# Performance work log

Hardware: AMD Instinct MI355X
Metric: run time of the kernel (lower is better)

## Reference

```python
import jax, jax.numpy as jnp
import numpy as np
from jax import lax

M, N, D = 4096, 4096, 256
SINKHORN_ITERATIONS = 100
SINKHORN_EPSILON = 0.1
DESC_SCALE = 0.05  # keep exp(S/eps) finite for random descriptors


def setup_inputs() -> dict:
    key = jax.random.key(0)
    k1, k2 = jax.random.split(key)
    d_M_q = jax.random.normal(k1, (M, D), dtype=jnp.float32) * DESC_SCALE
    d_N_r = jax.random.normal(k2, (N, D), dtype=jnp.float32) * DESC_SCALE
    z = jnp.float32(0.5)  # SuperGlue bin_score default
    return {"d_M_q": d_M_q, "d_N_r": d_N_r, "z": z}


def reference(d_M_q, d_N_r, z):
    m, n = d_M_q.shape[0], d_N_r.shape[0]
    # score matrix [M, N]
    S = jnp.einsum('md,nd->mn', d_M_q, d_N_r)
    # augment with dustbin row/col filled with z -> [M+1, N+1]
    dtype = d_M_q.dtype
    last_col = jnp.full((m, 1), z, dtype=dtype)
    last_row = jnp.full((1, n + 1), z, dtype=dtype)
    S_aug = jnp.concatenate([jnp.concatenate([S, last_col], axis=1), last_row], axis=0)
    K = jnp.exp(S_aug / SINKHORN_EPSILON)

    def step(K, _):
        K = K / K.sum(axis=1, keepdims=True)  # row normalize
        K = K / K.sum(axis=0, keepdims=True)  # col normalize
        return K, None

    K, _ = lax.scan(step, K, None, length=SINKHORN_ITERATIONS)
    P = K[:m, :n]
    return P, K
```

## Files before the change

### kernel.cpp

```cpp
#include <hip/hip_runtime.h>
#include <hip/hip_bf16.h>


#define MROWS 4096
#define NCOLS 4096
#define DDIM 256
#define MP1 4097
#define INV_EPS 10.0f
#define NBLK 256
#define XSLOT 4160
#define BAR_DW 160

typedef __attribute__((ext_vector_type(8))) short bf16x8;
typedef __attribute__((ext_vector_type(4))) float f32x4;
typedef __attribute__((ext_vector_type(2))) float f32x2;
typedef __attribute__((ext_vector_type(4))) unsigned short u16x4;

static __device__ __forceinline__ unsigned short f2bf(float f) {
  __hip_bfloat16 h = __float2bfloat16(f);
  union { __hip_bfloat16 h; unsigned short s; } c;
  c.h = h;
  return c.s;
}

static __device__ __forceinline__ void ld_strip(const float* ps, float4& xv) {
  asm volatile("global_load_dwordx4 %0, %1, off sc0 sc1\n\t"
               "s_waitcnt vmcnt(0)"
               : "=v"(xv) : "v"(ps) : "memory");
}
static __device__ __forceinline__ void ld_strip_dust(const float* ps, const float* pd,
                                                     float4& xv, float& xd) {
  asm volatile("global_load_dwordx4 %0, %2, off sc0 sc1\n\t"
               "global_load_dword %1, %3, off sc0 sc1\n\t"
               "s_waitcnt vmcnt(0)"
               : "=v"(xv), "=v"(xd)
               : "v"(ps), "v"(pd)
               : "memory");
}
static __device__ __forceinline__ void st_coherent(float* p, float x) {
  asm volatile("global_store_dword %0, %1, off sc0 sc1" :: "v"(p), "v"(x) : "memory");
}
static __device__ __forceinline__ unsigned ld_flagc(const unsigned* p) {
  unsigned r;
  asm volatile("global_load_dword %0, %1, off sc0 sc1\n\t"
               "s_waitcnt vmcnt(0)"
               : "=v"(r) : "v"(p) : "memory");
  return r;
}
static __device__ __forceinline__ void st_flag(unsigned* p, unsigned x) {
  asm volatile("global_store_dword %0, %1, off sc0 sc1" :: "v"(p), "v"(x) : "memory");
}

template <int MODE>
__global__ __launch_bounds__(256) void mfma_gemm_kernel(
    const float* __restrict__ Q, const float* __restrict__ R,
    unsigned char* __restrict__ A8, unsigned char* __restrict__ T8,
    float* __restrict__ Kf, float* __restrict__ P,
    const float* __restrict__ u, const float* __restrict__ v)
{
  __shared__ unsigned short Qs[128][40];
  __shared__ unsigned short Rs[128][40];

  const int tid = threadIdx.x;
  const int lane = tid & 63;
  const int wid = tid >> 6;
  const int wy = wid >> 1;
  const int wx = wid & 1;
  const int rb = blockIdx.y * 128;
  const int cb = blockIdx.x * 128;
  const int lr = tid >> 3;
  const int lf = (tid & 7) * 4;

  f32x4 acc[4][4];
#pragma unroll
  for (int m = 0; m < 4; ++m)
#pragma unroll
    for (int n = 0; n < 4; ++n)
      acc[m][n] = (f32x4){0.f, 0.f, 0.f, 0.f};

  for (int k0 = 0; k0 < DDIM; k0 += 32) {
    float4 qv[4], rv[4];
#pragma unroll
    for (int i = 0; i < 4; ++i) {
      qv[i] = *reinterpret_cast<const float4*>(&Q[(size_t)(rb + lr + 32 * i) * DDIM + k0 + lf]);
      rv[i] = *reinterpret_cast<const float4*>(&R[(size_t)(cb + lr + 32 * i) * DDIM + k0 + lf]);
    }
    __syncthreads();
#pragma unroll
    for (int i = 0; i < 4; ++i) {
      u16x4 qs = {f2bf(qv[i].x), f2bf(qv[i].y), f2bf(qv[i].z), f2bf(qv[i].w)};
      u16x4 rs = {f2bf(rv[i].x), f2bf(rv[i].y), f2bf(rv[i].z), f2bf(rv[i].w)};
      *reinterpret_cast<u16x4*>(&Qs[lr + 32 * i][lf]) = qs;
      *reinterpret_cast<u16x4*>(&Rs[lr + 32 * i][lf]) = rs;
    }
    __syncthreads();

    const int ko = (lane >> 4) * 8;
    const int fr = lane & 15;
    bf16x8 af[4], bg[4];
#pragma unroll
    for (int m = 0; m < 4; ++m)
      af[m] = *reinterpret_cast<const bf16x8*>(&Qs[wy * 64 + m * 16 + fr][ko]);
#pragma unroll
    for (int n = 0; n < 4; ++n)
      bg[n] = *reinterpret_cast<const bf16x8*>(&Rs[wx * 64 + n * 16 + fr][ko]);
#pragma unroll
    for (int m = 0; m < 4; ++m)
#pragma unroll
      for (int n = 0; n < 4; ++n)
        acc[m][n] = __builtin_amdgcn_mfma_f32_16x16x32_bf16(af[m], bg[n], acc[m][n], 0, 0, 0);
  }

  const int r0 = (lane >> 4) * 4;
  const int fc = lane & 15;
#pragma unroll
  for (int m = 0; m < 4; ++m) {
    const int row0 = rb + wy * 64 + m * 16 + r0;
    float uu[4];
    if (MODE == 1) {
#pragma unroll
      for (int r = 0; r < 4; ++r) uu[r] = u[row0 + r];
    }
#pragma unroll
    for (int n = 0; n < 4; ++n) {
      const int col = cb + wx * 64 + n * 16 + fc;
      if (MODE == 0) {
        float kv[4];
#pragma unroll
        for (int r = 0; r < 4; ++r) kv[r] = __expf(acc[m][n][r] * INV_EPS);
        int packed = __builtin_amdgcn_cvt_pk_fp8_f32(kv[0], kv[1], 0, false);
        packed = __builtin_amdgcn_cvt_pk_fp8_f32(kv[2], kv[3], packed, true);
        *reinterpret_cast<unsigned int*>(&T8[(size_t)col * NCOLS + row0]) = (unsigned int)packed;
#pragma unroll
        for (int r = 0; r < 4; ++r)
          A8[(size_t)(row0 + r) * NCOLS + col] = (unsigned char)(((unsigned int)packed >> (8 * r)) & 0xffu);
      } else {
        const float vc = v[col];
#pragma unroll
        for (int r = 0; r < 4; ++r) {
          const float kv = __expf(acc[m][n][r] * INV_EPS);
          const float val = uu[r] * kv * vc;
          Kf[(size_t)(row0 + r) * MP1 + col] = val;
          P[(size_t)(row0 + r) * NCOLS + col] = val;
        }
      }
    }
  }
}

__global__ void init_sync_kernel(float* __restrict__ xbuf, unsigned* __restrict__ bar)
{
  const int i = blockIdx.x * 1024 + threadIdx.x;
  if (i < MP1) xbuf[i] = 1.0f;
  if (i < BAR_DW) bar[i] = 0u;
}

__global__ void edgeK_kernel(const float* __restrict__ zp, float* __restrict__ Kf,
                             const float* __restrict__ u, const float* __restrict__ v)
{
  const int i = blockIdx.x * 256 + threadIdx.x;
  if (i >= MP1) return;
  const float E = __expf(zp[0] * INV_EPS);
  Kf[(size_t)i * MP1 + NCOLS] = u[i] * E * v[NCOLS];
  Kf[(size_t)MROWS * MP1 + i] = u[MROWS] * E * v[i];
}

__global__ __launch_bounds__(1024) void sinkhorn_persist_kernel(
    const unsigned char* __restrict__ A8, const unsigned char* __restrict__ T8,
    float* __restrict__ xbuf, const float* __restrict__ zp,
    unsigned* __restrict__ bar)
{
  __shared__ unsigned char lA[16 * 4096];
  __shared__ unsigned char lT[16 * 4096];
  __shared__ float scratch[2][16][17];
  __shared__ float dscr[2][16];

  const int tid = threadIdx.x;
  const int b = blockIdx.x;
  const int lane = tid & 63;
  const int w = tid >> 6;
  const float E = __expf(zp[0] * INV_EPS);
  const int rev4 = ((lane & 1) << 3) | ((lane & 2) << 1) | ((lane & 4) >> 1) | ((lane & 8) >> 3);

  unsigned* cg = bar + ((b & 7) << 4);
  unsigned* release = bar + 128;

  {
    const uint4* gA = reinterpret_cast<const uint4*>(A8 + (size_t)b * 16 * 4096);
    const uint4* gT = reinterpret_cast<const uint4*>(T8 + (size_t)b * 16 * 4096);
    uint4* sA = reinterpret_cast<uint4*>(lA);
    uint4* sT = reinterpret_cast<uint4*>(lT);
#pragma unroll
    for (int i = 0; i < 4; ++i) {
      sA[tid + 1024 * i] = gA[tid + 1024 * i];
      sT[tid + 1024 * i] = gT[tid + 1024 * i];
    }
  }
  __syncthreads();

  const int c0 = (w << 8) + (lane << 2);

  for (int g = 1; g <= 200; ++g) {
    const unsigned char* Kl = (g & 1) ? lA : lT;
    const float* xin = xbuf + (size_t)((g - 1) & 3) * XSLOT;
    float* xout = xbuf + (size_t)(g & 3) * XSLOT;
    const unsigned need = (unsigned)(g - 1);
    const int sb = g & 1;

    if (w == 0) {
      unsigned fv = ld_flagc(release + (lane & 7));
      while (!__all((int)(fv >= need))) {
        __builtin_amdgcn_s_sleep(1);
        fv = ld_flagc(release + (lane & 7));
      }
    }
    __syncthreads();

    float4 xv; float xd = 0.f;
    if (w == 0) ld_strip_dust(xin + c0, xin + 4096, xv, xd);
    else        ld_strip(xin + c0, xv);

    float acc[16];
#pragma unroll
    for (int r = 0; r < 16; ++r) {
      const unsigned int aw = *reinterpret_cast<const unsigned int*>(Kl + r * 4096 + c0);
      const f32x2 lo = __builtin_amdgcn_cvt_pk_f32_fp8((int)aw, false);
      const f32x2 hi = __builtin_amdgcn_cvt_pk_f32_fp8((int)aw, true);
      acc[r] = lo.x * xv.x + lo.y * xv.y + hi.x * xv.z + hi.y * xv.w;
    }

    float r8[8], r4[4], r2[2], r1;
    {
      const bool f0 = (lane & 1) != 0;
#pragma unroll
      for (int k = 0; k < 8; ++k) {
        const float send = f0 ? acc[k] : acc[k + 8];
        const float keep = f0 ? acc[k + 8] : acc[k];
        r8[k] = keep + __shfl_xor(send, 1, 64);
      }
      const bool f1 = (lane & 2) != 0;
#pragma unroll
      for (int k = 0; k < 4; ++k) {
        const float send = f1 ? r8[k] : r8[k + 4];
        const float keep = f1 ? r8[k + 4] : r8[k];
        r4[k] = keep + __shfl_xor(send, 2, 64);
      }
      const bool f2 = (lane & 4) != 0;
#pragma unroll
      for (int k = 0; k < 2; ++k) {
        const float send = f2 ? r4[k] : r4[k + 2];
        const float keep = f2 ? r4[k + 2] : r4[k];
        r2[k] = keep + __shfl_xor(send, 4, 64);
      }
      const bool f3 = (lane & 8) != 0;
      {
        const float send = f3 ? r2[0] : r2[1];
        const float keep = f3 ? r2[1] : r2[0];
        r1 = keep + __shfl_xor(send, 8, 64);
      }
      r1 += __shfl_xor(r1, 16, 64);
      r1 += __shfl_xor(r1, 32, 64);
    }
    if (lane < 16) scratch[sb][rev4][w] = r1;

    if (b == 0) {
      float sv = xv.x + xv.y + xv.z + xv.w;
      sv += __shfl_xor(sv, 1, 64);  sv += __shfl_xor(sv, 2, 64);
      sv += __shfl_xor(sv, 4, 64);  sv += __shfl_xor(sv, 8, 64);
      sv += __shfl_xor(sv, 16, 64); sv += __shfl_xor(sv, 32, 64);
      if (lane == 0) dscr[sb][w] = sv;
    }
    __syncthreads();

    if (w == 0) {
      const int rr = lane >> 2, wq = (lane & 3) * 4;
      float s = scratch[sb][rr][wq] + scratch[sb][rr][wq + 1]
              + scratch[sb][rr][wq + 2] + scratch[sb][rr][wq + 3];
      s += __shfl_xor(s, 1, 64);
      s += __shfl_xor(s, 2, 64);
      if ((lane & 3) == 0)
        st_coherent(xout + (b << 4) + rr, 1.0f / (s + E * xd));
      if (b == 0) {
        float t = (lane < 16) ? dscr[sb][lane] : 0.f;
        t += __shfl_xor(t, 1, 64);  t += __shfl_xor(t, 2, 64);
        t += __shfl_xor(t, 4, 64);  t += __shfl_xor(t, 8, 64);
        t += __shfl_xor(t, 16, 64); t += __shfl_xor(t, 32, 64);
        if (lane == 0) st_coherent(xout + 4096, 1.0f / (E * (t + xd)));
      }
      asm volatile("s_waitcnt vmcnt(0)" ::: "memory");
      if (lane == 0) {
        const unsigned a = __hip_atomic_fetch_add(cg, 1u, __ATOMIC_RELAXED,
                                                  __HIP_MEMORY_SCOPE_AGENT);
        if (a == 32u * (unsigned)g - 1u)
          st_flag(release + (b & 7), (unsigned)g);
      }
    }
  }
}

extern "C" void kernel_launch(void* const* d_in, const int* in_sizes, int n_in,
                              void* d_out, int out_size, void* d_ws, size_t ws_size,
                              hipStream_t stream) {
  const float* Q = (const float*)d_in[0];
  const float* R = (const float*)d_in[1];
  const float* z = (const float*)d_in[2];

  float* P = (float*)d_out;
  float* Kf = P + (size_t)MROWS * NCOLS;

  unsigned char* A8 = (unsigned char*)d_ws;
  unsigned char* T8 = A8 + (size_t)MROWS * NCOLS;
  float* xbuf = (float*)(T8 + (size_t)MROWS * NCOLS);
  unsigned* bar = (unsigned*)(xbuf + (size_t)4 * XSLOT);

  const float* u_final = xbuf + (size_t)3 * XSLOT;
  const float* v_final = xbuf;

  mfma_gemm_kernel<0><<<dim3(32, 32), 256, 0, stream>>>(Q, R, A8, T8, nullptr, nullptr, nullptr, nullptr);
  init_sync_kernel<<<5, 1024, 0, stream>>>(xbuf, bar);
  sinkhorn_persist_kernel<<<NBLK, 1024, 0, stream>>>(A8, T8, xbuf, z, bar);
  mfma_gemm_kernel<1><<<dim3(32, 32), 256, 0, stream>>>(Q, R, nullptr, nullptr, Kf, P, u_final, v_final);
  edgeK_kernel<<<(MP1 + 255) / 256, 256, 0, stream>>>(z, Kf, u_final, v_final);
}
```

Measured before the change: 924.3 us.

## Use per-iteration scaling slots, relax load coherence, vectorize scaling-vector stores

The four-slot ring for the Sinkhorn scaling vectors is replaced by 201 distinct slots, one per half-iteration. Since no slot is ever rewritten, the strip loads can drop the sc1 bit, and the init kernel zero-fills every slot. Each block packs its 16 outputs into four dwordx4 coherent stores instead of 16 scalar stores, and prewarms the output lines early. This aims to shorten the per-iteration latency on the grid-barrier critical path, at the cost of a larger workspace and a bigger init kernel.

```diff
diff --git a/kernel.cpp b/kernel.cpp
--- a/kernel.cpp
+++ b/kernel.cpp
@@ -9,6 +9,7 @@
 #define INV_EPS 10.0f
 #define NBLK 256
 #define XSLOT 4160
+#define NSLOT 201
 #define BAR_DW 160
 
 typedef __attribute__((ext_vector_type(8))) short bf16x8;
@@ -23,15 +24,15 @@
   return c.s;
 }
 
-static __device__ __forceinline__ void ld_strip(const float* ps, float4& xv) {
-  asm volatile("global_load_dwordx4 %0, %1, off sc0 sc1\n\t"
+static __device__ __forceinline__ void ld_strip(const float* ps, f32x4& xv) {
+  asm volatile("global_load_dwordx4 %0, %1, off sc0\n\t"
                "s_waitcnt vmcnt(0)"
                : "=v"(xv) : "v"(ps) : "memory");
 }
 static __device__ __forceinline__ void ld_strip_dust(const float* ps, const float* pd,
-                                                     float4& xv, float& xd) {
-  asm volatile("global_load_dwordx4 %0, %2, off sc0 sc1\n\t"
-               "global_load_dword %1, %3, off sc0 sc1\n\t"
+                                                     f32x4& xv, float& xd) {
+  asm volatile("global_load_dwordx4 %0, %2, off sc0\n\t"
+               "global_load_dword %1, %3, off sc0\n\t"
                "s_waitcnt vmcnt(0)"
                : "=v"(xv), "=v"(xd)
                : "v"(ps), "v"(pd)
@@ -39,6 +40,9 @@
 }
 static __device__ __forceinline__ void st_coherent(float* p, float x) {
   asm volatile("global_store_dword %0, %1, off sc0 sc1" :: "v"(p), "v"(x) : "memory");
+}
+static __device__ __forceinline__ void st16_coherent(float* p, f32x4 x) {
+  asm volatile("global_store_dwordx4 %0, %1, off sc0 sc1" :: "v"(p), "v"(x) : "memory");
 }
 static __device__ __forceinline__ unsigned ld_flagc(const unsigned* p) {
   unsigned r;
@@ -49,6 +53,10 @@
 }
 static __device__ __forceinline__ void st_flag(unsigned* p, unsigned x) {
   asm volatile("global_store_dword %0, %1, off sc0 sc1" :: "v"(p), "v"(x) : "memory");
+}
+static __device__ __forceinline__ void prewarm(const float* p) {
+  float r;
+  asm volatile("global_load_dword %0, %1, off sc0 sc1" : "=v"(r) : "v"(p) : "memory");
 }
 
 template <int MODE>
@@ -151,7 +159,7 @@
 __global__ void init_sync_kernel(float* __restrict__ xbuf, unsigned* __restrict__ bar)
 {
   const int i = blockIdx.x * 1024 + threadIdx.x;
-  if (i < MP1) xbuf[i] = 1.0f;
+  if (i < NSLOT * XSLOT) xbuf[i] = (i < XSLOT) ? 1.0f : 0.0f;
   if (i < BAR_DW) bar[i] = 0u;
 }
 
@@ -202,8 +210,8 @@
 
   for (int g = 1; g <= 200; ++g) {
     const unsigned char* Kl = (g & 1) ? lA : lT;
-    const float* xin = xbuf + (size_t)((g - 1) & 3) * XSLOT;
-    float* xout = xbuf + (size_t)(g & 3) * XSLOT;
+    const float* xin = xbuf + (size_t)(g - 1) * XSLOT;
+    float* xout = xbuf + (size_t)g * XSLOT;
     const unsigned need = (unsigned)(g - 1);
     const int sb = g & 1;
 
@@ -216,9 +224,12 @@
     }
     __syncthreads();
 
-    float4 xv; float xd = 0.f;
+    f32x4 xv; float xd = 0.f;
     if (w == 0) ld_strip_dust(xin + c0, xin + 4096, xv, xd);
     else        ld_strip(xin + c0, xv);
+
+    if (w == 0 && lane == 0) prewarm(xout + (b << 4));
+    if (w == 0 && b == 0 && lane == 1) prewarm(xout + 4096);
 
     float acc[16];
 #pragma unroll
@@ -278,8 +289,14 @@
               + scratch[sb][rr][wq + 2] + scratch[sb][rr][wq + 3];
       s += __shfl_xor(s, 1, 64);
       s += __shfl_xor(s, 2, 64);
-      if ((lane & 3) == 0)
-        st_coherent(xout + (b << 4) + rr, 1.0f / (s + E * xd));
+      const float sf = 1.0f / (s + E * xd);
+      const int sl = (lane & 3) << 4;
+      f32x4 o;
+      o.x = __shfl(sf, sl + 0, 64);
+      o.y = __shfl(sf, sl + 4, 64);
+      o.z = __shfl(sf, sl + 8, 64);
+      o.w = __shfl(sf, sl + 12, 64);
+      if (lane < 4) st16_coherent(xout + (b << 4) + lane * 4, o);
       if (b == 0) {
         float t = (lane < 16) ? dscr[sb][lane] : 0.f;
         t += __shfl_xor(t, 1, 64);  t += __shfl_xor(t, 2, 64);
@@ -311,13 +328,13 @@
   unsigned char* A8 = (unsigned char*)d_ws;
   unsigned char* T8 = A8 + (size_t)MROWS * NCOLS;
   float* xbuf = (float*)(T8 + (size_t)MROWS * NCOLS);
-  unsigned* bar = (unsigned*)(xbuf + (size_t)4 * XSLOT);
-
-  const float* u_final = xbuf + (size_t)3 * XSLOT;
-  const float* v_final = xbuf;
+  unsigned* bar = (unsigned*)(xbuf + (size_t)NSLOT * XSLOT);
+
+  const float* u_final = xbuf + (size_t)199 * XSLOT;
+  const float* v_final = xbuf + (size_t)200 * XSLOT;
 
   mfma_gemm_kernel<0><<<dim3(32, 32), 256, 0, stream>>>(Q, R, A8, T8, nullptr, nullptr, nullptr, nullptr);
-  init_sync_kernel<<<5, 1024, 0, stream>>>(xbuf, bar);
+  init_sync_kernel<<<817, 1024, 0, stream>>>(xbuf, bar);
   sinkhorn_persist_kernel<<<NBLK, 1024, 0, stream>>>(A8, T8, xbuf, z, bar);
   mfma_gemm_kernel<1><<<dim3(32, 32), 256, 0, stream>>>(Q, R, nullptr, nullptr, Kf, P, u_final, v_final);
   edgeK_kernel<<<(MP1 + 255) / 256, 256, 0, stream>>>(z, Kf, u_final, v_final);
```

Result: no change. 930.5 us (+0.7%).
